# Performance work log

Hardware: AMD Instinct MI355X
Metric: run time of the kernel (lower is better)

Reference implementation:

```python
import jax, jax.numpy as jnp
import numpy as np
jax.config.update('jax_enable_x64', True)

N = 64
NX = N * N
BATCH = 32
EPS = 0.1
N_ITER = 25
SCHUR_REG = 1e-9
BIG = 1e10


def _constraints(group_ids, exposure):
    """Build shared equality system A z = b (doubly-stochastic + fairness row).
    Matches torch code which uses A = A[0] (first batch element only)."""
    ROW = jnp.kron(jnp.eye(N, dtype=jnp.float64), jnp.ones((1, N), dtype=jnp.float64))  # row sums
    COL = jnp.kron(jnp.ones((1, N), dtype=jnp.float64), jnp.eye(N, dtype=jnp.float64))  # col sums
    g = group_ids[0].astype(jnp.float64)                       # [N]
    f = g / g.sum() - (1.0 - g) / (1.0 - g).sum()              # group contrast
    fair = (f[:, None] * exposure.astype(jnp.float64)[None, :]).reshape(1, NX)  # entry i*N+j = f_i * expo_j
    A = jnp.concatenate([ROW, COL, fair], axis=0)              # [2N+1, NX]
    b = jnp.concatenate([jnp.ones(2 * N, dtype=jnp.float64), jnp.zeros(1, dtype=jnp.float64)])
    return A, b


def _solve_qp(p, A, b):
    """Batched primal-dual interior point for min 0.5*eps*||z||^2 + p'z
    s.t. A z = b, 0 <= z <= 1. G=[-I;I] structure is exploited: G'DG is diagonal,
    so each Newton step reduces to a small [neq,neq] Schur solve (as in qpth)."""
    B, nx = p.shape
    neq = A.shape[0]
    m = 2 * nx
    h = jnp.concatenate([jnp.zeros(nx, dtype=p.dtype), jnp.ones(nx, dtype=p.dtype)])
    eye_neq = jnp.eye(neq, dtype=p.dtype)

    def step(carry, _):
        z, y, s, lam = carry
        s1, s2 = s[:, :nx], s[:, nx:]
        l1, l2 = lam[:, :nx], lam[:, nx:]
        Gz = jnp.concatenate([-z, z], axis=1)
        r_dual = EPS * z + p + y @ A + (-l1 + l2)          # Qz + p + A'y + G'lam
        r_eq = z @ A.T - b                                  # A z - b
        r_ineq = Gz + s - h                                 # G z + s - h
        mu = jnp.sum(s * lam, axis=1, keepdims=True) / m
        r_cent = lam * s - 0.1 * mu                         # sigma = 0.1 centering
        tmp = (lam * r_ineq - r_cent) / s                   # [B, 2nx]
        rhs_z = -(r_dual + (-tmp[:, :nx] + tmp[:, nx:]))
        invD = 1.0 / (EPS + l1 / s1 + l2 / s2)              # (Q + G'DG)^{-1} diagonal
        S = jnp.einsum('ik,bk,jk->bij', A, invD, A) + SCHUR_REG * eye_neq
        rhs_y = (rhs_z * invD) @ A.T + r_eq
        dy = jnp.linalg.solve(S, rhs_y[..., None])[..., 0]
        dz = (rhs_z - dy @ A) * invD
        ds = -r_ineq - jnp.concatenate([-dz, dz], axis=1)
        dlam = (-r_cent - lam * ds) / s
        # fraction-to-boundary step length (grad-safe division)
        den_s = jnp.where(ds < 0, ds, -1.0)
        den_l = jnp.where(dlam < 0, dlam, -1.0)
        a_s = jnp.where(ds < 0, -s / den_s, BIG).min(axis=1)
        a_l = jnp.where(dlam < 0, -lam / den_l, BIG).min(axis=1)
        alpha = jnp.minimum(1.0, 0.99 * jnp.minimum(a_s, a_l))[:, None]
        return (z + alpha * dz, y + alpha * dy, s + alpha * ds, lam + alpha * dlam), None

    init = (jnp.zeros_like(p), jnp.zeros((B, neq), p.dtype),
            jnp.ones((B, m), p.dtype), jnp.ones((B, m), p.dtype))
    (z, _, _, _), _ = jax.lax.scan(step, init, None, length=N_ITER)
    return z


def setup_inputs() -> dict:
    key = jax.random.key(0)
    k1, k2 = jax.random.split(key)
    x = jax.random.normal(k1, (BATCH, NX), dtype=jnp.float32)
    gid = jax.random.randint(k2, (BATCH, N), 0, 2).astype(jnp.float32)
    # guarantee both groups present (avoid division by zero in f)
    gid = gid.at[:, 0].set(1.0).at[:, 1].set(0.0)
    exposure = (1.0 / jnp.log2(jnp.arange(N, dtype=jnp.float32) + 2.0))  # position_bias_vector[:N]
    return {"x": x, "group_ids": gid, "exposure": exposure}


def reference(x, group_ids, exposure):
    A, b = _constraints(group_ids, exposure)
    p = x.astype(jnp.float64)
    z = _solve_qp(p, A, b)
    return z.reshape(-1, N, N).astype(jnp.float32)
```

## Files before the change

kernel.cpp:

```cpp
#include <hip/hip_runtime.h>
#include <math.h>

#define NN    64
#define NXX   4096
#define NT    512
#define NCH   8
#define NITER 25
#define EPSQ  0.1
#define SREG  1e-9
#define BIGV  1e10

__device__ __forceinline__ double wsum(double v) {
#pragma unroll
  for (int m = 32; m > 0; m >>= 1) v += __shfl_xor(v, m, 64);
  return v;
}
__device__ __forceinline__ double wmin(double v) {
#pragma unroll
  for (int m = 32; m > 0; m >>= 1) v = fmin(v, __shfl_xor(v, m, 64));
  return v;
}
__device__ __forceinline__ double wmax(double v) {
#pragma unroll
  for (int m = 32; m > 0; m >>= 1) v = fmax(v, __shfl_xor(v, m, 64));
  return v;
}

#define F1_INVERT(K0)                                                         \
  {                                                                           \
    const int r_ = lane >> 2, q_ = lane & 3;                                  \
    double Brow[4];                                                           \
    _Pragma("unroll")                                                         \
    for (int e = 0; e < 4; ++e) Brow[e] = Mg[(K0) + r_][(K0) + ((e << 2) | q_)]; \
    _Pragma("unroll")                                                         \
    for (int t = 0; t < 16; ++t) {                                            \
      const int et = t >> 2, qt = t & 3;                                      \
      double pm  = __shfl(Brow[et], (r_ << 2) | qt, 64);                      \
      double pv  = __shfl(Brow[et], (t << 2) | qt, 64);                       \
      double pr0 = __shfl(Brow[0], (t << 2) | q_, 64);                        \
      double pr1 = __shfl(Brow[1], (t << 2) | q_, 64);                        \
      double pr2 = __shfl(Brow[2], (t << 2) | q_, 64);                        \
      double pr3 = __shfl(Brow[3], (t << 2) | q_, 64);                        \
      double ip = __builtin_amdgcn_rcp(pv);                                   \
      ip = ip * (2.0 - pv * ip);                                              \
      ip = ip * (2.0 - pv * ip);                                              \
      double ps0 = pr0 * ip, ps1 = pr1 * ip, ps2 = pr2 * ip, ps3 = pr3 * ip;  \
      if (r_ == t) {                                                          \
        Brow[0] = ps0; Brow[1] = ps1; Brow[2] = ps2; Brow[3] = ps3;           \
        if (q_ == qt) Brow[et] = ip;                                          \
      } else {                                                                \
        Brow[0] -= pm * ps0; Brow[1] -= pm * ps1;                             \
        Brow[2] -= pm * ps2; Brow[3] -= pm * ps3;                             \
        if (q_ == qt) Brow[et] = -pm * ip;                                    \
      }                                                                       \
    }                                                                         \
    _Pragma("unroll")                                                         \
    for (int e = 0; e < 4; ++e) Binv[r_][(e << 2) | q_] = Brow[e];            \
  }

__device__ __forceinline__ void pair_jl(int idx, int& j, int& l) {
  j = (int)((1.0 + sqrt(8.0 * (double)idx + 1.0)) * 0.5);
  while (j * (j - 1) / 2 > idx) --j;
  while ((j + 1) * j / 2 <= idx) ++j;
  l = idx - j * (j - 1) / 2;
}

__global__ __launch_bounds__(NT, 2)
void ipm_kernel(const float* __restrict__ xin, const float* __restrict__ gidin,
                const float* __restrict__ expin, float* __restrict__ outp)
{
  const int b    = blockIdx.x;
  const int tid  = threadIdx.x;
  const int lane = tid & 63;
  const int w    = tid >> 6;

  __shared__ double DnT[64][65];
  __shared__ double Mg[64][67];
  __shared__ double Pbuf[16][52];
  __shared__ double Binv[16][18];
  __shared__ double cpZ[8][64], cpA[8][64], cpB[8][64], cpC[8][64];
  __shared__ double rhs1[64], rhs2v[64];
  __shared__ double Rhv[64], Ruv[64], ccv[64], wvv[64];
  __shared__ double usv[64], rsv[64], uvv[64], mw0[64];
  __shared__ double yav[64], ydv[64];
  __shared__ double fvec[64], evec[64];
  __shared__ double wpFz[8], wpMu[8], wpQ[8], wpFg[8], wpS[8], wpL[8];
  __shared__ double scal[8];

  if (tid < 64) {
    fvec[tid] = (double)gidin[tid];
    evec[tid] = (double)expin[tid];
    yav[tid] = 0.0; ydv[tid] = 0.0;
  }
  if (tid == 0) scal[6] = 0.0;
  __syncthreads();
  if (tid == 0) {
    double gs = 0.0;
    for (int i = 0; i < 64; ++i) gs += fvec[i];
    scal[7] = gs;
  }
  __syncthreads();
  if (tid < 64) {
    double g = fvec[tid], gs = scal[7];
    fvec[tid] = g / gs - (1.0 - g) / (64.0 - gs);
  }
  __syncthreads();

  double p[NCH], z[NCH], s1[NCH], s2[NCH], l1[NCH], l2[NCH], fe[NCH];
  const double ev = evec[lane];
#pragma unroll
  for (int k = 0; k < NCH; ++k) {
    int e = tid + NT * k;
    p[k]  = (double)xin[(size_t)b * NXX + e];
    z[k] = 0.0; s1[k] = 1.0; s2[k] = 1.0; l1[k] = 1.0; l2[k] = 1.0;
    fe[k] = fvec[w + 8 * k] * ev;
  }

  for (int iter = 0; iter < NITER; ++iter) {
    double rq1[NCH];
    double cz = 0.0, fz = 0.0, msl = 0.0;
#pragma unroll
    for (int k = 0; k < NCH; ++k) {
      rq1[k] = wsum(z[k]) - 1.0;
      cz  += z[k];
      fz  += fe[k] * z[k];
      msl += s1[k] * l1[k] + s2[k] * l2[k];
    }
    cpZ[w][lane] = cz;
    {
      double a = wsum(fz), c = wsum(msl);
      if (lane == 0) { wpFz[w] = a; wpMu[w] = c; }
    }
    __syncthreads();

    double mu8 = 0.0;
#pragma unroll
    for (int q = 0; q < 8; ++q) mu8 += wpMu[q];
    const double mu01 = 0.1 * (mu8 / 8192.0);
    const double yt   = scal[6];
    double dinv[NCH], rz[NCH], is1[NCH], is2[NCH];
    double cD = 0.0, cfD = 0.0, cg = 0.0, qac = 0.0, fgac = 0.0;
#pragma unroll
    for (int k = 0; k < NCH; ++k) {
      int i = w + 8 * k;
      is1[k] = 1.0 / s1[k];  is2[k] = 1.0 / s2[k];
      double D = 1.0 / (EPSQ + l1[k] * is1[k] + l2[k] * is2[k]);
      dinv[k] = D;
      double rd  = EPSQ * z[k] + p[k] + (yav[i] + ydv[lane] + yt * fe[k]) + (l2[k] - l1[k]);
      double tt1 = (mu01 - l1[k] * z[k]) * is1[k];
      double tt2 = (l2[k] * (z[k] - 1.0) + mu01) * is2[k];
      double r = -(rd - tt1 + tt2);
      rz[k] = r;
      double g = r * D;
      double sD  = wsum(D);
      double sED = wsum(ev * D);
      double sg  = wsum(g);
      double Rh  = sD + SREG;
      if (lane == 0) {
        Rhv[i]  = Rh;
        Ruv[i]  = sED;
        rhs1[i] = sg + rq1[k];
      }
      DnT[lane][i] = D * rsqrt(Rh);
      cD  += D;  cfD += fvec[i] * D;  cg += g;
      qac += fe[k] * fe[k] * D;
      fgac += fe[k] * g;
    }
    cpA[w][lane] = cD; cpB[w][lane] = cfD; cpC[w][lane] = cg;
    {
      double a = wsum(qac), c = wsum(fgac);
      if (lane == 0) { wpQ[w] = a; wpFg[w] = c; }
    }
    __syncthreads();

    if (tid < 64) {
      double sZ = 0.0, sA = 0.0, sB = 0.0, sC = 0.0;
#pragma unroll
      for (int q = 0; q < 8; ++q) {
        sZ += cpZ[q][tid]; sA += cpA[q][tid]; sB += cpB[q][tid]; sC += cpC[q][tid];
      }
      ccv[tid]   = sA;
      wvv[tid]   = evec[tid] * sB;
      rhs2v[tid] = sC + sZ - 1.0;
      double ir  = rsqrt(Rhv[tid]);
      double u   = fvec[tid] * Ruv[tid];
      uvv[tid] = u;
      usv[tid] = u * ir;
      rsv[tid] = rhs1[tid] * ir;
    }
    __syncthreads();

    if (tid < 272) {
      int R = 0;
#pragma unroll
      for (int r = 1; r < 16; ++r) if (tid >= r * (33 - r)) R = r;
      const int C  = 2 * R + (tid - R * (33 - R));
      const int r0 = R << 2, c0 = C << 1;
      double m00=0.0,m01=0.0,m10=0.0,m11=0.0,m20=0.0,m21=0.0,m30=0.0,m31=0.0;
#pragma unroll 4
      for (int i = 0; i < 64; ++i) {
        double a0 = DnT[r0+0][i], a1 = DnT[r0+1][i];
        double a2 = DnT[r0+2][i], a3 = DnT[r0+3][i];
        double b0v = DnT[c0+0][i], b1v = DnT[c0+1][i];
        m00 += a0*b0v; m01 += a0*b1v;
        m10 += a1*b0v; m11 += a1*b1v;
        m20 += a2*b0v; m21 += a2*b1v;
        m30 += a3*b0v; m31 += a3*b1v;
      }
      Mg[r0+0][c0+0] = ((r0+0)==(c0+0) ? ccv[r0+0]+SREG : 0.0) - m00;
      Mg[r0+0][c0+1] = ((r0+0)==(c0+1) ? ccv[r0+0]+SREG : 0.0) - m01;
      Mg[r0+1][c0+0] = ((r0+1)==(c0+0) ? ccv[r0+1]+SREG : 0.0) - m10;
      Mg[r0+1][c0+1] = ((r0+1)==(c0+1) ? ccv[r0+1]+SREG : 0.0) - m11;
      Mg[r0+2][c0+0] = ((r0+2)==(c0+0) ? ccv[r0+2]+SREG : 0.0) - m20;
      Mg[r0+2][c0+1] = ((r0+2)==(c0+1) ? ccv[r0+2]+SREG : 0.0) - m21;
      Mg[r0+3][c0+0] = ((r0+3)==(c0+0) ? ccv[r0+3]+SREG : 0.0) - m30;
      Mg[r0+3][c0+1] = ((r0+3)==(c0+1) ? ccv[r0+3]+SREG : 0.0) - m31;
    } else if (tid < 400) {
      const int d = tid - 272;
      const int j = d & 63, cc = d >> 6;
      double acc = 0.0;
#pragma unroll 8
      for (int i = 0; i < 64; ++i) {
        double vv = cc ? usv[i] : rsv[i];
        acc += DnT[j][i] * vv;
      }
      if (cc == 0) Mg[j][64] = rhs2v[j] - acc;
      else { double vv2 = wvv[j] - acc; Mg[j][65] = vv2; mw0[j] = vv2; }
    }
    __syncthreads();

    if (w == 0) {
#pragma unroll
      for (int e = 0; e < 2; ++e) {
        int idx = 2 * lane + e;
        if (idx < 120) { int j, l; pair_jl(idx, j, l); Mg[j][l] = Mg[l][j]; }
      }
      F1_INVERT(0);
    } else {
      const int wtid = tid - 64;
#pragma unroll
      for (int r = 0; r < 5; ++r) {
        int idx = 120 + wtid + 448 * r;
        if (idx < 2016) { int j, l; pair_jl(idx, j, l); Mg[j][l] = Mg[l][j]; }
      }
    }
    __syncthreads();

#pragma unroll
    for (int pk = 0; pk < 4; ++pk) {
      const int k0   = 16 * pk;
      const int rest = 50 - k0;

      for (int o = tid; o < 16 * rest; o += NT) {
        int t = o / rest, c = o - t * rest;
        double acc = 0.0;
#pragma unroll
        for (int s = 0; s < 16; ++s) acc += Binv[t][s] * Mg[k0 + s][k0 + 16 + c];
        Pbuf[t][c] = acc;
      }
      __syncthreads();

      if (pk < 3) {
        if (w == 0) {
#pragma unroll
          for (int e = 0; e < 4; ++e) {
            int idx = lane + 64 * e;
            int r = k0 + 16 + (idx >> 4), c = (idx & 15);
            double acc = Mg[r][k0 + 16 + c];
#pragma unroll
            for (int t = 0; t < 16; ++t) acc -= Mg[r][k0 + t] * Pbuf[t][c];
            Mg[r][k0 + 16 + c] = acc;
          }
          F1_INVERT(k0 + 16);
        } else {
          const int wtid = tid - 64;
          for (int o = wtid; o < 48 * rest; o += 448) {
            int rr = o / rest, c = o - rr * rest;
            int r = rr < k0 ? rr : rr + 16;
            bool excl = (r >= k0 + 16) && (r < k0 + 32) && (c < 16);
            if (!excl) {
              double acc = Mg[r][k0 + 16 + c];
#pragma unroll
              for (int t = 0; t < 16; ++t) acc -= Mg[r][k0 + t] * Pbuf[t][c];
              Mg[r][k0 + 16 + c] = acc;
            }
          }
          for (int o = wtid; o < 16 * rest; o += 448) {
            int t = o / rest, c = o - t * rest;
            Mg[k0 + t][k0 + 16 + c] = Pbuf[t][c];
          }
        }
      } else {
        for (int o = tid; o < 48 * rest; o += NT) {
          int rr = o / rest, c = o - rr * rest;
          int r = rr < k0 ? rr : rr + 16;
          double acc = Mg[r][k0 + 16 + c];
#pragma unroll
          for (int t = 0; t < 16; ++t) acc -= Mg[r][k0 + t] * Pbuf[t][c];
          Mg[r][k0 + 16 + c] = acc;
        }
        for (int o = tid; o < 16 * rest; o += NT) {
          int t = o / rest, c = o - t * rest;
          Mg[k0 + t][k0 + 16 + c] = Pbuf[t][c];
        }
      }
      __syncthreads();
    }

    double ddl, tf;
    {
      double qsum = 0.0, fg = 0.0, fzs = 0.0;
#pragma unroll
      for (int q = 0; q < 8; ++q) { qsum += wpQ[q]; fg += wpFg[q]; fzs += wpFz[q]; }
      double h1 = Mg[lane][64], h2 = Mg[lane][65];
      double a1 = wsum(usv[lane] * usv[lane]);
      double a2 = wsum(usv[lane] * rsv[lane]);
      double a3 = wsum(mw0[lane] * h1);
      double a4 = wsum(mw0[lane] * h2);
      double qp  = qsum + SREG - a1;
      double r3p = (fg + fzs) - a2;
      tf  = (r3p - a3) / (qp - a4);
      ddl = h1 - tf * h2;
    }

    double dar[NCH];
    double bs = 0.0;
    double rl = BIGV;
#pragma unroll
    for (int k = 0; k < NCH; ++k) {
      int i = w + 8 * k;
      double rdot = wsum(dinv[k] * ddl);
      double dv = (rhs1[i] - rdot - uvv[i] * tf) / Rhv[i];
      dar[k] = dv;
      double d   = (rz[k] - (dv + ddl + tf * fe[k])) * dinv[k];
      double ds1 = d - (s1[k] - z[k]);
      double ds2 = -(z[k] + s2[k] - 1.0) - d;
      bs = fmax(bs, fmax(-ds1 * is1[k], -ds2 * is2[k]));
      double dl1 = (-(l1[k] * s1[k] - mu01) - l1[k] * ds1) * is1[k];
      double dl2 = (-(l2[k] * s2[k] - mu01) - l2[k] * ds2) * is2[k];
      if (dl1 < 0.0) rl = fmin(rl, -l1[k] / dl1);
      if (dl2 < 0.0) rl = fmin(rl, -l2[k] / dl2);
    }
    bs = wmax(bs);
    rl = wmin(rl);
    if (lane == 0) { wpS[w] = bs; wpL[w] = rl; }
    __syncthreads();
    double al;
    {
      double bm = wpS[0], rm = wpL[0];
#pragma unroll
      for (int q = 1; q < 8; ++q) { bm = fmax(bm, wpS[q]); rm = fmin(rm, wpL[q]); }
      double a_s = bm > 0.0 ? 1.0 / bm : BIGV;
      al = fmin(1.0, 0.99 * fmin(a_s, rm));
    }

#pragma unroll
    for (int k = 0; k < NCH; ++k) {
      double d   = (rz[k] - (dar[k] + ddl + tf * fe[k])) * dinv[k];
      double ds1 = d - (s1[k] - z[k]);
      double ds2 = -(z[k] + s2[k] - 1.0) - d;
      double dl1 = (-(l1[k] * s1[k] - mu01) - l1[k] * ds1) * is1[k];
      double dl2 = (-(l2[k] * s2[k] - mu01) - l2[k] * ds2) * is2[k];
      z[k]  += al * d;
      s1[k] += al * ds1;
      s2[k] += al * ds2;
      l1[k] += al * dl1;
      l2[k] += al * dl2;
      if (lane == 0) yav[w + 8 * k] += al * dar[k];
    }
    if (tid < 64) ydv[tid] += al * ddl;
    if (tid == 0) scal[6] += al * tf;
  }

#pragma unroll
  for (int k = 0; k < NCH; ++k) {
    int e = tid + NT * k;
    outp[(size_t)b * NXX + e] = (float)z[k];
  }
}

extern "C" void kernel_launch(void* const* d_in, const int* in_sizes, int n_in,
                              void* d_out, int out_size, void* d_ws, size_t ws_size,
                              hipStream_t stream)
{
  const float* x   = (const float*)d_in[0];
  const float* gid = (const float*)d_in[1];
  const float* ex  = (const float*)d_in[2];
  float* out = (float*)d_out;
  int nb = in_sizes[0] / NXX;
  hipLaunchKernelGGL(ipm_kernel, dim3(nb), dim3(NT), 0, stream, x, gid, ex, out);
}
```

Baseline: 1.295 ms.

## Double block size to 1024 threads and repartition Schur-complement work

Raises threads per block from 512 to 1024 (16 waves), halving per-thread element chunks, and remaps the Gram-matrix build so each of 544 threads computes a 4x1 tile instead of 272 threads computing 4x2. Strided loops for symmetrization and block elimination are updated to the larger thread count. The aim is more latency hiding and shorter serial phases within each batch block, since only 32 blocks run. The cost is more shared-memory reduction slots, a larger per-block register budget, and a dropped 2-blocks-per-CU launch bound.

After: 1.474 ms. +13.8%, slower.

```diff
diff --git a/kernel.cpp b/kernel.cpp
--- a/kernel.cpp
+++ b/kernel.cpp
@@ -3,8 +3,9 @@
 
 #define NN    64
 #define NXX   4096
-#define NT    512
-#define NCH   8
+#define NT    1024
+#define NW    16
+#define NCH   4
 #define NITER 25
 #define EPSQ  0.1
 #define SREG  1e-9
@@ -65,7 +66,7 @@
   l = idx - j * (j - 1) / 2;
 }
 
-__global__ __launch_bounds__(NT, 2)
+__global__ __launch_bounds__(NT)
 void ipm_kernel(const float* __restrict__ xin, const float* __restrict__ gidin,
                 const float* __restrict__ expin, float* __restrict__ outp)
 {
@@ -78,13 +79,13 @@
   __shared__ double Mg[64][67];
   __shared__ double Pbuf[16][52];
   __shared__ double Binv[16][18];
-  __shared__ double cpZ[8][64], cpA[8][64], cpB[8][64], cpC[8][64];
+  __shared__ double cpZ[NW][64], cpA[NW][64], cpB[NW][64], cpC[NW][64];
   __shared__ double rhs1[64], rhs2v[64];
   __shared__ double Rhv[64], Ruv[64], ccv[64], wvv[64];
   __shared__ double usv[64], rsv[64], uvv[64], mw0[64];
   __shared__ double yav[64], ydv[64];
   __shared__ double fvec[64], evec[64];
-  __shared__ double wpFz[8], wpMu[8], wpQ[8], wpFg[8], wpS[8], wpL[8];
+  __shared__ double wpFz[NW], wpMu[NW], wpQ[NW], wpFg[NW], wpS[NW], wpL[NW];
   __shared__ double scal[8];
 
   if (tid < 64) {
@@ -113,7 +114,7 @@
     int e = tid + NT * k;
     p[k]  = (double)xin[(size_t)b * NXX + e];
     z[k] = 0.0; s1[k] = 1.0; s2[k] = 1.0; l1[k] = 1.0; l2[k] = 1.0;
-    fe[k] = fvec[w + 8 * k] * ev;
+    fe[k] = fvec[w + NW * k] * ev;
   }
 
   for (int iter = 0; iter < NITER; ++iter) {
@@ -135,14 +136,14 @@
 
     double mu8 = 0.0;
 #pragma unroll
-    for (int q = 0; q < 8; ++q) mu8 += wpMu[q];
+    for (int q = 0; q < NW; ++q) mu8 += wpMu[q];
     const double mu01 = 0.1 * (mu8 / 8192.0);
     const double yt   = scal[6];
     double dinv[NCH], rz[NCH], is1[NCH], is2[NCH];
     double cD = 0.0, cfD = 0.0, cg = 0.0, qac = 0.0, fgac = 0.0;
 #pragma unroll
     for (int k = 0; k < NCH; ++k) {
-      int i = w + 8 * k;
+      int i = w + NW * k;
       is1[k] = 1.0 / s1[k];  is2[k] = 1.0 / s2[k];
       double D = 1.0 / (EPSQ + l1[k] * is1[k] + l2[k] * is2[k]);
       dinv[k] = D;
@@ -176,7 +177,7 @@
     if (tid < 64) {
       double sZ = 0.0, sA = 0.0, sB = 0.0, sC = 0.0;
 #pragma unroll
-      for (int q = 0; q < 8; ++q) {
+      for (int q = 0; q < NW; ++q) {
         sZ += cpZ[q][tid]; sA += cpA[q][tid]; sB += cpB[q][tid]; sC += cpC[q][tid];
       }
       ccv[tid]   = sA;
@@ -190,33 +191,27 @@
     }
     __syncthreads();
 
-    if (tid < 272) {
+    if (tid < 544) {
       int R = 0;
 #pragma unroll
-      for (int r = 1; r < 16; ++r) if (tid >= r * (33 - r)) R = r;
-      const int C  = 2 * R + (tid - R * (33 - R));
-      const int r0 = R << 2, c0 = C << 1;
-      double m00=0.0,m01=0.0,m10=0.0,m11=0.0,m20=0.0,m21=0.0,m30=0.0,m31=0.0;
-#pragma unroll 4
+      for (int r = 1; r < 16; ++r) if (tid >= (64 * r - 2 * r * (r - 1))) R = r;
+      const int c  = 4 * R + (tid - (64 * R - 2 * R * (R - 1)));
+      const int r0 = R << 2;
+      double m0 = 0.0, m1 = 0.0, m2 = 0.0, m3 = 0.0;
+#pragma unroll 8
       for (int i = 0; i < 64; ++i) {
-        double a0 = DnT[r0+0][i], a1 = DnT[r0+1][i];
-        double a2 = DnT[r0+2][i], a3 = DnT[r0+3][i];
-        double b0v = DnT[c0+0][i], b1v = DnT[c0+1][i];
-        m00 += a0*b0v; m01 += a0*b1v;
-        m10 += a1*b0v; m11 += a1*b1v;
-        m20 += a2*b0v; m21 += a2*b1v;
-        m30 += a3*b0v; m31 += a3*b1v;
-      }
-      Mg[r0+0][c0+0] = ((r0+0)==(c0+0) ? ccv[r0+0]+SREG : 0.0) - m00;
-      Mg[r0+0][c0+1] = ((r0+0)==(c0+1) ? ccv[r0+0]+SREG : 0.0) - m01;
-      Mg[r0+1][c0+0] = ((r0+1)==(c0+0) ? ccv[r0+1]+SREG : 0.0) - m10;
-      Mg[r0+1][c0+1] = ((r0+1)==(c0+1) ? ccv[r0+1]+SREG : 0.0) - m11;
-      Mg[r0+2][c0+0] = ((r0+2)==(c0+0) ? ccv[r0+2]+SREG : 0.0) - m20;
-      Mg[r0+2][c0+1] = ((r0+2)==(c0+1) ? ccv[r0+2]+SREG : 0.0) - m21;
-      Mg[r0+3][c0+0] = ((r0+3)==(c0+0) ? ccv[r0+3]+SREG : 0.0) - m30;
-      Mg[r0+3][c0+1] = ((r0+3)==(c0+1) ? ccv[r0+3]+SREG : 0.0) - m31;
-    } else if (tid < 400) {
-      const int d = tid - 272;
+        double bv = DnT[c][i];
+        m0 += DnT[r0 + 0][i] * bv;
+        m1 += DnT[r0 + 1][i] * bv;
+        m2 += DnT[r0 + 2][i] * bv;
+        m3 += DnT[r0 + 3][i] * bv;
+      }
+      Mg[r0 + 0][c] = ((r0 + 0) == c ? ccv[c] + SREG : 0.0) - m0;
+      Mg[r0 + 1][c] = ((r0 + 1) == c ? ccv[c] + SREG : 0.0) - m1;
+      Mg[r0 + 2][c] = ((r0 + 2) == c ? ccv[c] + SREG : 0.0) - m2;
+      Mg[r0 + 3][c] = ((r0 + 3) == c ? ccv[c] + SREG : 0.0) - m3;
+    } else if (tid < 672) {
+      const int d = tid - 544;
       const int j = d & 63, cc = d >> 6;
       double acc = 0.0;
 #pragma unroll 8
@@ -239,8 +234,8 @@
     } else {
       const int wtid = tid - 64;
 #pragma unroll
-      for (int r = 0; r < 5; ++r) {
-        int idx = 120 + wtid + 448 * r;
+      for (int r = 0; r < 2; ++r) {
+        int idx = 120 + wtid + 960 * r;
         if (idx < 2016) { int j, l; pair_jl(idx, j, l); Mg[j][l] = Mg[l][j]; }
       }
     }
@@ -274,7 +269,7 @@
           F1_INVERT(k0 + 16);
         } else {
           const int wtid = tid - 64;
-          for (int o = wtid; o < 48 * rest; o += 448) {
+          for (int o = wtid; o < 48 * rest; o += 960) {
             int rr = o / rest, c = o - rr * rest;
             int r = rr < k0 ? rr : rr + 16;
             bool excl = (r >= k0 + 16) && (r < k0 + 32) && (c < 16);
@@ -285,7 +280,7 @@
               Mg[r][k0 + 16 + c] = acc;
             }
           }
-          for (int o = wtid; o < 16 * rest; o += 448) {
+          for (int o = wtid; o < 16 * rest; o += 960) {
             int t = o / rest, c = o - t * rest;
             Mg[k0 + t][k0 + 16 + c] = Pbuf[t][c];
           }
@@ -311,7 +306,7 @@
     {
       double qsum = 0.0, fg = 0.0, fzs = 0.0;
 #pragma unroll
-      for (int q = 0; q < 8; ++q) { qsum += wpQ[q]; fg += wpFg[q]; fzs += wpFz[q]; }
+      for (int q = 0; q < NW; ++q) { qsum += wpQ[q]; fg += wpFg[q]; fzs += wpFz[q]; }
       double h1 = Mg[lane][64], h2 = Mg[lane][65];
       double a1 = wsum(usv[lane] * usv[lane]);
       double a2 = wsum(usv[lane] * rsv[lane]);
@@ -328,7 +323,7 @@
     double rl = BIGV;
 #pragma unroll
     for (int k = 0; k < NCH; ++k) {
-      int i = w + 8 * k;
+      int i = w + NW * k;
       double rdot = wsum(dinv[k] * ddl);
       double dv = (rhs1[i] - rdot - uvv[i] * tf) / Rhv[i];
       dar[k] = dv;
@@ -349,7 +344,7 @@
     {
       double bm = wpS[0], rm = wpL[0];
 #pragma unroll
-      for (int q = 1; q < 8; ++q) { bm = fmax(bm, wpS[q]); rm = fmin(rm, wpL[q]); }
+      for (int q = 1; q < NW; ++q) { bm = fmax(bm, wpS[q]); rm = fmin(rm, wpL[q]); }
       double a_s = bm > 0.0 ? 1.0 / bm : BIGV;
       al = fmin(1.0, 0.99 * fmin(a_s, rm));
     }
@@ -366,7 +361,7 @@
       s2[k] += al * ds2;
       l1[k] += al * dl1;
       l2[k] += al * dl2;
-      if (lane == 0) yav[w + 8 * k] += al * dar[k];
+      if (lane == 0) yav[w + NW * k] += al * dar[k];
     }
     if (tid < 64) ydv[tid] += al * ddl;
     if (tid == 0) scal[6] += al * tf;
```
